# Kernel tuning notes

Hardware: AMD Instinct MI355X
Metric: run time of the kernel (lower is better)

## Reference

```python
import jax, jax.numpy as jnp
import numpy as np
from jax import lax

H_STEP = 1.0 / 3.0  # h = (t1 - t0) / N with t0=0, t1=1, N=3
N_STEPS = 3


def _conv(x, w):
    # x: [B, C, H, W], w: [O, I, kh, kw], 'same' padding, stride 1
    return lax.conv_general_dilated(
        x, w, window_strides=(1, 1), padding='SAME',
        dimension_numbers=('NCHW', 'OIHW', 'NCHW'))


def setup_inputs() -> dict:
    key = jax.random.key(0)
    ks = jax.random.split(key, 5)
    B, C, H, W = 16, 128, 128, 128
    fan_in = C * 9
    return {
        'x': jax.random.normal(ks[0], (B, C, H, W), dtype=jnp.float32),
        'w1': jax.random.normal(ks[1], (C, C, 3, 3), dtype=jnp.float32) * (2.0 / fan_in) ** 0.5,
        'b1': jax.random.normal(ks[2], (C,), dtype=jnp.float32) * 0.01,
        'w2': jax.random.normal(ks[3], (C, C, 3, 3), dtype=jnp.float32) * (2.0 / fan_in) ** 0.5,
        'b2': jax.random.normal(ks[4], (C,), dtype=jnp.float32) * 0.01,
    }


def reference(x, w1, b1, w2, b2):
    # Euler-step residual block: x <- x + h * conv2(relu(conv1(x))) for N steps
    for _ in range(N_STEPS):
        t = jax.nn.relu(_conv(x, w1) + b1[None, :, None, None])
        x = x + H_STEP * (_conv(t, w2) + b2[None, :, None, None])
    return jax.nn.relu(x)
```

## Files before the change

kernel.cpp:

```cpp
#include <hip/hip_runtime.h>
#include <hip/hip_bf16.h>


#define BATCH 16
#define CH    128
#define HH    128
#define WW    128
#define H_STEP (1.0f/3.0f)

typedef short bf16x8 __attribute__((ext_vector_type(8)));
typedef float f32x4  __attribute__((ext_vector_type(4)));

__device__ __forceinline__ float bf2f(unsigned short u) {
    union { unsigned int i; float f; } c; c.i = ((unsigned int)u) << 16; return c.f;
}
__device__ __forceinline__ unsigned short f2bf(float f) {
    union { float f; unsigned int i; } c; c.f = f;
    unsigned int i = c.i;
    return (unsigned short)((i + 0x7FFFu + ((i >> 16) & 1u)) >> 16);
}

__device__ __forceinline__ void gload16(const unsigned short* g, unsigned short* l) {
    __builtin_amdgcn_global_load_lds(
        (const __attribute__((address_space(1))) unsigned int*)g,
        (__attribute__((address_space(3))) unsigned int*)l, 16, 0, 0);
}

__global__ __launch_bounds__(256)
void transpose_x(const float* __restrict__ x, unsigned short* __restrict__ xb)
{
    __shared__ unsigned short s[128 * 132];
    const int tid = threadIdx.x;
    const int bz  = blockIdx.x;
    const int b = bz >> 7, y = bz & 127;

    #pragma unroll
    for (int it = 0; it < 16; ++it) {
        int idx = it * 256 + tid;
        int ci = idx >> 5, xq = idx & 31;
        float4 v = *(const float4*)&x[(((size_t)b * CH + ci) * HH + y) * WW + xq * 4];
        uint2 p;
        p.x = (unsigned int)f2bf(v.x) | ((unsigned int)f2bf(v.y) << 16);
        p.y = (unsigned int)f2bf(v.z) | ((unsigned int)f2bf(v.w) << 16);
        *(uint2*)&s[ci * 132 + xq * 4] = p;
    }
    __syncthreads();
    #pragma unroll
    for (int it = 0; it < 8; ++it) {
        int idx = it * 256 + tid;
        int xx = idx >> 4, cc = idx & 15;
        unsigned short t[8];
        #pragma unroll
        for (int k = 0; k < 8; ++k) t[k] = s[(cc * 8 + k) * 132 + xx];
        uint4 p;
        p.x = (unsigned int)t[0] | ((unsigned int)t[1] << 16);
        p.y = (unsigned int)t[2] | ((unsigned int)t[3] << 16);
        p.z = (unsigned int)t[4] | ((unsigned int)t[5] << 16);
        p.w = (unsigned int)t[6] | ((unsigned int)t[7] << 16);
        *(uint4*)&xb[((size_t)(b * HH + y) * WW + xx) * CH + cc * 8] = p;
    }
}

__global__ __launch_bounds__(256)
void convert_w(const float* __restrict__ w, unsigned short* __restrict__ wb)
{
    int idx = blockIdx.x * 256 + threadIdx.x;
    #pragma unroll
    for (int t = 0; t < 9; ++t)
        wb[t * 16384 + idx] = f2bf(w[(size_t)idx * 9 + t]);
}

template<int MODE>
__global__ __launch_bounds__(256, 3)
void conv_mfma(const unsigned short* __restrict__ in,
               const unsigned short* __restrict__ wb,
               const float* __restrict__ bias,
               const unsigned short* resb,
               unsigned short* outb,
               float* __restrict__ outf)
{
    __shared__ unsigned short s_in[130 * CH];
    __shared__ unsigned short s_w [2][128 * 32];

    const int tid = threadIdx.x;
    const int bz0 = blockIdx.x;
    const int bz  = ((bz0 & 7) << 8) | (bz0 >> 3);
    const int b = bz >> 7, y = bz & 127;

    const int lane = tid & 63;
    const int wid  = tid >> 6;
    const int woc0 = (wid >> 1) * 64;
    const int wpx0 = (wid & 1) * 64;
    const int n16  = lane & 15;
    const int q    = lane >> 4;

    const int wrow4 = lane >> 2;
    const int wslot = lane & 3;
    const int xl    = lane >> 4;
    const int ch16  = lane & 15;

    const int kylo = (y == 0)      ? 1 : 0;
    const int kyhi = (y == HH - 1) ? 1 : 2;
    const int NS   = (kyhi - kylo + 1) * 12;

    f32x4 acc[4][4];
    #pragma unroll
    for (int i = 0; i < 4; ++i)
        #pragma unroll
        for (int j = 0; j < 4; ++j) acc[i][j] = (f32x4)0.0f;

    if (tid < 32) {
        int r  = (tid < 16) ? 0 : 129;
        int cc = tid & 15;
        uint4 z = {0u, 0u, 0u, 0u};
        *(uint4*)&s_in[r * CH + cc * 8] = z;
    }

    auto stage_in = [&](int gy) {
        const size_t inrow = ((size_t)(b * HH + gy) * WW) * CH;
        #pragma unroll
        for (int c = 0; c < 8; ++c) {
            int x   = wid * 32 + c * 4 + xl;
            int swz = (x + 1) & 7;
            const unsigned short* src = in + inrow + (size_t)x * CH + ((ch16 ^ swz) << 3);
            unsigned short* dst = (unsigned short*)s_in + CH + (wid * 8 + c) * 512;
            gload16(src, dst);
        }
    };
    auto stage_w = [&](int tap, int kq, int buf) {
        const unsigned short* wt = wb + tap * 16384 + kq * 32;
        #pragma unroll
        for (int c = 0; c < 2; ++c) {
            int row = (wid * 2 + c) * 16 + wrow4;
            const unsigned short* src = wt + row * 128 + ((wslot ^ (row & 3)) << 3);
            unsigned short* dst = &s_w[buf][(wid * 2 + c) * 512];
            gload16(src, dst);
        }
    };

    stage_in(y + kylo - 1);
    stage_w(kylo * 3, 0, 0);
    __syncthreads();

    int kyi = 0, r12 = 0;
    for (int s = 0; s < NS; ++s) {
        const int cur = s & 1;
        const int kx  = r12 >> 2;
        const int kq  = r12 & 3;

        int r12n = r12 + 1, kyin = kyi;
        if (r12n == 12) { r12n = 0; ++kyin; }

        if (s + 1 < NS)
            stage_w((kylo + kyin) * 3 + (r12n >> 2), r12n & 3, cur ^ 1);

        {
            bf16x8 af[4], bfr[4];
            #pragma unroll
            for (int i = 0; i < 4; ++i) {
                int row = woc0 + i * 16 + n16;
                af[i] = *(const bf16x8*)&s_w[cur][row * 32 + ((q ^ (row & 3)) << 3)];
            }
            const int cqb = kq * 4 + q;
            #pragma unroll
            for (int j = 0; j < 4; ++j) {
                int rowb = wpx0 + j * 16 + n16 + kx;
                bfr[j] = *(const bf16x8*)&s_in[rowb * CH + ((cqb ^ (rowb & 7)) << 3)];
            }
            #pragma unroll
            for (int i = 0; i < 4; ++i)
                #pragma unroll
                for (int j = 0; j < 4; ++j)
                    acc[i][j] = __builtin_amdgcn_mfma_f32_16x16x32_bf16(
                        af[i], bfr[j], acc[i][j], 0, 0, 0);
        }

        if (r12 == 11 && s + 1 < NS) {
            __syncthreads();
            stage_in(y + kylo + kyi);
            __syncthreads();
        } else {
            __syncthreads();
        }
        r12 = r12n; kyi = kyin;
    }

    const int ybase = (b * HH + y) * WW;
    if (MODE == 0 || MODE == 1) {
        #pragma unroll
        for (int j = 0; j < 4; ++j) {
            int x = wpx0 + j * 16 + n16;
            size_t pbase = (size_t)(ybase + x) * CH;
            #pragma unroll
            for (int i = 0; i < 4; ++i) {
                int oc0 = woc0 + i * 16 + q * 4;
                float v0 = acc[i][j][0] + bias[oc0 + 0];
                float v1 = acc[i][j][1] + bias[oc0 + 1];
                float v2 = acc[i][j][2] + bias[oc0 + 2];
                float v3 = acc[i][j][3] + bias[oc0 + 3];
                if (MODE == 0) {
                    v0 = fmaxf(v0, 0.f); v1 = fmaxf(v1, 0.f);
                    v2 = fmaxf(v2, 0.f); v3 = fmaxf(v3, 0.f);
                } else {
                    uint2 rr = *(const uint2*)&resb[pbase + oc0];
                    v0 = bf2f((unsigned short)(rr.x & 0xffff)) + H_STEP * v0;
                    v1 = bf2f((unsigned short)(rr.x >> 16))    + H_STEP * v1;
                    v2 = bf2f((unsigned short)(rr.y & 0xffff)) + H_STEP * v2;
                    v3 = bf2f((unsigned short)(rr.y >> 16))    + H_STEP * v3;
                }
                uint2 po;
                po.x = (unsigned int)f2bf(v0) | ((unsigned int)f2bf(v1) << 16);
                po.y = (unsigned int)f2bf(v2) | ((unsigned int)f2bf(v3) << 16);
                *(uint2*)&outb[pbase + oc0] = po;
            }
        }
    } else {
        #pragma unroll
        for (int i = 0; i < 4; ++i) {
            #pragma unroll
            for (int r = 0; r < 4; ++r) {
                int oc = woc0 + i * 16 + q * 4 + r;
                float bv = bias[oc];
                size_t orow = ((size_t)(b * CH + oc) * HH + y) * WW;
                #pragma unroll
                for (int j = 0; j < 4; ++j) {
                    int x = wpx0 + j * 16 + n16;
                    float v = acc[i][j][r] + bv;
                    v = bf2f(resb[(size_t)(ybase + x) * CH + oc]) + H_STEP * v;
                    outf[orow + x] = fmaxf(v, 0.f);
                }
            }
        }
    }
}

extern "C" void kernel_launch(void* const* d_in, const int* in_sizes, int n_in,
                              void* d_out, int out_size, void* d_ws, size_t ws_size,
                              hipStream_t stream) {
    const float* x0 = (const float*)d_in[0];
    const float* w1 = (const float*)d_in[1];
    const float* b1 = (const float*)d_in[2];
    const float* w2 = (const float*)d_in[3];
    const float* b2 = (const float*)d_in[4];

    const size_t NELEM = (size_t)BATCH * CH * HH * WW;
    unsigned short* XB = (unsigned short*)d_ws;
    unsigned short* T  = XB + NELEM;

    unsigned short* WB1;
    if (ws_size >= NELEM * 4 + 2 * 294912)
        WB1 = T + NELEM;
    else
        WB1 = (unsigned short*)d_in[0];
    unsigned short* WB2 = WB1 + 9 * 16384;

    dim3 block(256);
    dim3 gridRow(BATCH * HH);

    transpose_x<<<gridRow, block, 0, stream>>>(x0, XB);
    convert_w<<<dim3(64), block, 0, stream>>>(w1, WB1);
    convert_w<<<dim3(64), block, 0, stream>>>(w2, WB2);

    conv_mfma<0><<<gridRow, block, 0, stream>>>(XB, WB1, b1, nullptr, T, nullptr);
    conv_mfma<1><<<gridRow, block, 0, stream>>>(T, WB2, b2, XB, XB, nullptr);
    conv_mfma<0><<<gridRow, block, 0, stream>>>(XB, WB1, b1, nullptr, T, nullptr);
    conv_mfma<1><<<gridRow, block, 0, stream>>>(T, WB2, b2, XB, XB, nullptr);
    conv_mfma<0><<<gridRow, block, 0, stream>>>(XB, WB1, b1, nullptr, T, nullptr);
    conv_mfma<2><<<gridRow, block, 0, stream>>>(T, WB2, b2, XB, nullptr, (float*)d_out);
}
```

Before: 797.6 us.

## Stream input row in channel quarters with triple-buffered weights and fine-grained waits

Replaces the full 130x128 input-row staging (which stalled the loop with a double barrier at each kernel-row boundary) with double-buffered 32-channel input slices reordered so the loop iterates kq outer and kx inner. Weights move to a triple buffer prefetched two steps ahead, and __syncthreads is replaced by explicit vmcnt waits plus s_barrier so async global-to-LDS loads overlap with the MFMAs. MFMA priority is raised with s_setprio. LDS use drops, which may allow more occupancy, but the hand-tuned waitcnt counts are fragile and the padding zeroing must stay correct for both buffers.

```diff
diff --git a/kernel.cpp b/kernel.cpp
--- a/kernel.cpp
+++ b/kernel.cpp
@@ -79,8 +79,8 @@
                unsigned short* outb,
                float* __restrict__ outf)
 {
-    __shared__ unsigned short s_in[130 * CH];
-    __shared__ unsigned short s_w [2][128 * 32];
+    __shared__ unsigned short s_is[2][130 * 32];
+    __shared__ unsigned short s_w [3][128 * 32];
 
     const int tid = threadIdx.x;
     const int bz0 = blockIdx.x;
@@ -94,14 +94,14 @@
     const int n16  = lane & 15;
     const int q    = lane >> 4;
 
-    const int wrow4 = lane >> 2;
-    const int wslot = lane & 3;
-    const int xl    = lane >> 4;
-    const int ch16  = lane & 15;
+    const int srow = lane >> 2;
+    const int slot = lane & 3;
 
     const int kylo = (y == 0)      ? 1 : 0;
     const int kyhi = (y == HH - 1) ? 1 : 2;
-    const int NS   = (kyhi - kylo + 1) * 12;
+    const int nky  = kyhi - kylo + 1;
+    const int NG   = nky * 4;
+    const int NS   = NG * 3;
 
     f32x4 acc[4][4];
     #pragma unroll
@@ -109,80 +109,77 @@
         #pragma unroll
         for (int j = 0; j < 4; ++j) acc[i][j] = (f32x4)0.0f;
 
-    if (tid < 32) {
-        int r  = (tid < 16) ? 0 : 129;
-        int cc = tid & 15;
-        uint4 z = {0u, 0u, 0u, 0u};
-        *(uint4*)&s_in[r * CH + cc * 8] = z;
-    }
-
-    auto stage_in = [&](int gy) {
-        const size_t inrow = ((size_t)(b * HH + gy) * WW) * CH;
-        #pragma unroll
-        for (int c = 0; c < 8; ++c) {
-            int x   = wid * 32 + c * 4 + xl;
-            int swz = (x + 1) & 7;
-            const unsigned short* src = in + inrow + (size_t)x * CH + ((ch16 ^ swz) << 3);
-            unsigned short* dst = (unsigned short*)s_in + CH + (wid * 8 + c) * 512;
-            gload16(src, dst);
-        }
-    };
     auto stage_w = [&](int tap, int kq, int buf) {
         const unsigned short* wt = wb + tap * 16384 + kq * 32;
         #pragma unroll
         for (int c = 0; c < 2; ++c) {
-            int row = (wid * 2 + c) * 16 + wrow4;
-            const unsigned short* src = wt + row * 128 + ((wslot ^ (row & 3)) << 3);
-            unsigned short* dst = &s_w[buf][(wid * 2 + c) * 512];
-            gload16(src, dst);
+            int row = (wid * 2 + c) * 16 + srow;
+            const unsigned short* src = wt + row * 128 + ((slot ^ (row & 3)) << 3);
+            gload16(src, &s_w[buf][(wid * 2 + c) * 512]);
         }
     };
-
-    stage_in(y + kylo - 1);
-    stage_w(kylo * 3, 0, 0);
-    __syncthreads();
-
-    int kyi = 0, r12 = 0;
+    auto stage_is = [&](int gy, int kq, int buf) {
+        const size_t inrow = ((size_t)(b * HH + gy) * WW) * CH + kq * 32;
+        #pragma unroll
+        for (int c = 0; c < 2; ++c) {
+            int r   = (c * 4 + wid) * 16 + srow;
+            int swz = (r + 1) & 3;
+            const unsigned short* src = in + inrow + (size_t)r * CH + ((slot ^ swz) << 3);
+            gload16(src, &s_is[buf][((c * 4 + wid) * 16 + 1) * 32]);
+        }
+    };
+
+    stage_w(kylo * 3 + 0, 0, 0);
+    stage_is(y + kylo - 1, 0, 0);
+    stage_w(kylo * 3 + 1, 0, 1);
+    if (tid < 16) {
+        int bfi = tid >> 3, rr = ((tid >> 2) & 1) ? 129 : 0, cc = tid & 3;
+        uint4 z = {0u, 0u, 0u, 0u};
+        *(uint4*)&s_is[bfi][rr * 32 + cc * 8] = z;
+    }
+    asm volatile("s_waitcnt lgkmcnt(0)" ::: "memory");
+
+    const int NSm1 = NS - 1;
     for (int s = 0; s < NS; ++s) {
-        const int cur = s & 1;
-        const int kx  = r12 >> 2;
-        const int kq  = r12 & 3;
-
-        int r12n = r12 + 1, kyin = kyi;
-        if (r12n == 12) { r12n = 0; ++kyin; }
-
-        if (s + 1 < NS)
-            stage_w((kylo + kyin) * 3 + (r12n >> 2), r12n & 3, cur ^ 1);
+        const int g   = s / 3;
+        const int kx  = s - g * 3;
+        const int kyi = g >> 2;
+        const int ig  = g & 1;
+
+        if (kx == 0) asm volatile("s_waitcnt vmcnt(2)" ::: "memory");
+        else         asm volatile("s_waitcnt vmcnt(4)" ::: "memory");
+        asm volatile("s_barrier" ::: "memory");
 
         {
-            bf16x8 af[4], bfr[4];
+            int wb2 = (kx == 0) ? 2 : (kx - 1);
+            int s2  = s + 2; if (s2 > NSm1) s2 = NSm1;
+            int g2  = s2 / 3, kx2 = s2 - g2 * 3;
+            stage_w((kylo + (g2 >> 2)) * 3 + kx2, g2 & 3, wb2);
+        }
+        if (kx == 0) {
+            int gn = g + 1; if (gn > NG - 1) gn = NG - 1;
+            stage_is(y + kylo + (gn >> 2) - 1, gn & 3, (g + 1) & 1);
+        }
+
+        bf16x8 af[4], bfr[4];
+        #pragma unroll
+        for (int i = 0; i < 4; ++i) {
+            int row = woc0 + i * 16 + n16;
+            af[i] = *(const bf16x8*)&s_w[kx][row * 32 + ((q ^ (row & 3)) << 3)];
+        }
+        #pragma unroll
+        for (int j = 0; j < 4; ++j) {
+            int rowb = wpx0 + j * 16 + n16 + kx;
+            bfr[j] = *(const bf16x8*)&s_is[ig][rowb * 32 + ((q ^ (rowb & 3)) << 3)];
+        }
+        __builtin_amdgcn_s_setprio(1);
+        #pragma unroll
+        for (int i = 0; i < 4; ++i)
             #pragma unroll
-            for (int i = 0; i < 4; ++i) {
-                int row = woc0 + i * 16 + n16;
-                af[i] = *(const bf16x8*)&s_w[cur][row * 32 + ((q ^ (row & 3)) << 3)];
-            }
-            const int cqb = kq * 4 + q;
-            #pragma unroll
-            for (int j = 0; j < 4; ++j) {
-                int rowb = wpx0 + j * 16 + n16 + kx;
-                bfr[j] = *(const bf16x8*)&s_in[rowb * CH + ((cqb ^ (rowb & 7)) << 3)];
-            }
-            #pragma unroll
-            for (int i = 0; i < 4; ++i)
-                #pragma unroll
-                for (int j = 0; j < 4; ++j)
-                    acc[i][j] = __builtin_amdgcn_mfma_f32_16x16x32_bf16(
-                        af[i], bfr[j], acc[i][j], 0, 0, 0);
-        }
-
-        if (r12 == 11 && s + 1 < NS) {
-            __syncthreads();
-            stage_in(y + kylo + kyi);
-            __syncthreads();
-        } else {
-            __syncthreads();
-        }
-        r12 = r12n; kyi = kyin;
+            for (int j = 0; j < 4; ++j)
+                acc[i][j] = __builtin_amdgcn_mfma_f32_16x16x32_bf16(
+                    af[i], bfr[j], acc[i][j], 0, 0, 0);
+        __builtin_amdgcn_s_setprio(0);
     }
 
     const int ybase = (b * HH + y) * WW;
```

Result: slower. 823.0 us (+3.2%).
